# Kernel tuning notes

Measured on AMD Instinct MI355X. Metric: run time of the kernel, lower is better.

Reference implementation:

```python
import jax, jax.numpy as jnp
import numpy as np

B, S1, S2, H = 8, 2048, 2048, 1024

def setup_inputs() -> dict:
    key = jax.random.key(0)
    k1, k2, k3, k4, k5, k6 = jax.random.split(key, 6)
    value = jax.random.normal(k1, (B, S1, H), dtype=jnp.float32)
    key_t = jax.random.normal(k2, (B, S2, H), dtype=jnp.float32)
    query = jax.random.normal(k3, (B, S1, H), dtype=jnp.float32)
    mask = jax.random.randint(k4, (B, S1, S2), 0, 2).astype(jnp.bool_)
    # Linear(hidden, hidden) params, torch default init scale
    bound = 1.0 / np.sqrt(H)
    W = jax.random.uniform(k5, (H, H), minval=-bound, maxval=bound, dtype=jnp.float32)
    b = jax.random.uniform(k6, (H,), minval=-bound, maxval=bound, dtype=jnp.float32)
    return {"value": value, "key": key_t, "query": query, "mask": mask, "W": W, "b": b}

def reference(value, key, query, mask, W, b):
    # q_proj = query @ W^T + b  (torch Linear)
    q_proj = jnp.einsum('bqh,oh->bqo', query, W) + b            # [B,S1,H]
    attn = jnp.einsum('bqh,bkh->bqk', q_proj, key)               # [B,S1,S2]
    attn = jnp.where(mask, -jnp.inf, attn)
    attn = jnp.transpose(attn, (0, 2, 1))                        # [B,S2,S1]
    weights = jax.nn.softmax(attn, axis=-1)                      # softmax over S1
    context = jnp.einsum('bks,bsh->bkh', weights, value)         # [B,S2,H]
    return context, weights
```

## Files before the change

kernel.cpp:

```cpp
#include <hip/hip_runtime.h>

#define B_  8
#define S1_ 2048
#define S2_ 2048
#define H_  1024

typedef unsigned short u16;
typedef __attribute__((ext_vector_type(8))) short short8;
typedef __attribute__((ext_vector_type(4))) float f32x4;

__device__ __forceinline__ float b2f(u16 u) {
  union { unsigned int i; float f; } v; v.i = ((unsigned int)u) << 16; return v.f;
}
__device__ __forceinline__ u16 f2b(float f) {
  union { float f; unsigned int i; } v; v.f = f;
  unsigned int r = v.i + 0x7fffu + ((v.i >> 16) & 1u);
  return (u16)(r >> 16);
}

__device__ __forceinline__ int swz(int row, int kk) {
  return (row * 32 + kk) ^ (((row >> 1) & 3) << 3);
}

__device__ __forceinline__ void cvt8_split(float4 va, float4 vb, short8* hi, short8* lo) {
  float x[8] = {va.x, va.y, va.z, va.w, vb.x, vb.y, vb.z, vb.w};
  short8 h, l;
#pragma unroll
  for (int e = 0; e < 8; ++e) {
    u16 hb = f2b(x[e]);
    h[e] = (short)hb;
    l[e] = (short)f2b(x[e] - b2f(hb));
  }
  *hi = h; *lo = l;
}
__device__ __forceinline__ short8 cvt8(float4 va, float4 vb) {
  float x[8] = {va.x, va.y, va.z, va.w, vb.x, vb.y, vb.z, vb.w};
  short8 h;
#pragma unroll
  for (int e = 0; e < 8; ++e) h[e] = (short)f2b(x[e]);
  return h;
}

template<bool ADD_BIAS, bool DO_MASK, bool SPLIT, bool BTR>
__global__ __launch_bounds__(256)
void gemm_k(const float* __restrict__ A, long sA,
            const float* __restrict__ B, long sB, int ldb,
            const float* __restrict__ bias,
            const int* __restrict__ mask, long sMask, int mask_ld,
            float* __restrict__ C, long sC, int ldc, int K)
{
  __shared__ __align__(16) union {
    u16 tile[SPLIT ? 4 : 2][128 * 32];
    unsigned char m[128][128];
  } sh;

  const int t    = threadIdx.x;
  const int lane = t & 63;
  const int wv   = t >> 6;
  const int wm   = wv >> 1, wn = wv & 1;
  const int batch = blockIdx.z;
  const int m0 = blockIdx.x * 128;
  const int n0 = blockIdx.y * 128;

  const float* Ab = A + (long)batch * sA + (long)m0 * K;
  const float* Bb = B + (long)batch * sB + (BTR ? (long)n0 : (long)n0 * ldb);

  f32x4 acc[4][4];
#pragma unroll
  for (int i = 0; i < 4; ++i)
#pragma unroll
    for (int j = 0; j < 4; ++j)
      acc[i][j] = (f32x4){0.f, 0.f, 0.f, 0.f};

  const int c0 = t,       r0 = c0 >> 2, o0 = (c0 & 3) * 8;
  const int c1 = t + 256, r1 = c1 >> 2, o1 = (c1 & 3) * 8;

  const int fr = lane & 15;
  const int kg = lane >> 4;

  for (int kc = 0; kc < K; kc += 32) {
    float4 a00 = *(const float4*)(Ab + (long)r0 * K + kc + o0);
    float4 a01 = *(const float4*)(Ab + (long)r0 * K + kc + o0 + 4);
    float4 a10 = *(const float4*)(Ab + (long)r1 * K + kc + o1);
    float4 a11 = *(const float4*)(Ab + (long)r1 * K + kc + o1 + 4);
    float4 bb[4];
    float btv[2][8];
    if (BTR) {
#pragma unroll
      for (int p = 0; p < 2; ++p)
#pragma unroll
        for (int e = 0; e < 8; ++e)
          btv[p][e] = Bb[(long)(kc + wv * 8 + e) * ldb + lane + p * 64];
    } else {
      bb[0] = *(const float4*)(Bb + (long)r0 * ldb + kc + o0);
      bb[1] = *(const float4*)(Bb + (long)r0 * ldb + kc + o0 + 4);
      bb[2] = *(const float4*)(Bb + (long)r1 * ldb + kc + o1);
      bb[3] = *(const float4*)(Bb + (long)r1 * ldb + kc + o1 + 4);
    }
    __syncthreads();

    if (SPLIT) {
      short8 h, l;
      cvt8_split(a00, a01, &h, &l);
      *(short8*)&sh.tile[0][swz(r0, o0)] = h;  *(short8*)&sh.tile[2][swz(r0, o0)] = l;
      cvt8_split(a10, a11, &h, &l);
      *(short8*)&sh.tile[0][swz(r1, o1)] = h;  *(short8*)&sh.tile[2][swz(r1, o1)] = l;
      cvt8_split(bb[0], bb[1], &h, &l);
      *(short8*)&sh.tile[1][swz(r0, o0)] = h;  *(short8*)&sh.tile[3][swz(r0, o0)] = l;
      cvt8_split(bb[2], bb[3], &h, &l);
      *(short8*)&sh.tile[1][swz(r1, o1)] = h;  *(short8*)&sh.tile[3][swz(r1, o1)] = l;
    } else {
      *(short8*)&sh.tile[0][swz(r0, o0)] = cvt8(a00, a01);
      *(short8*)&sh.tile[0][swz(r1, o1)] = cvt8(a10, a11);
      if (BTR) {
#pragma unroll
        for (int p = 0; p < 2; ++p) {
          short8 h;
#pragma unroll
          for (int e = 0; e < 8; ++e) h[e] = (short)f2b(btv[p][e]);
          *(short8*)&sh.tile[1][swz(lane + p * 64, wv * 8)] = h;
        }
      } else {
        *(short8*)&sh.tile[1][swz(r0, o0)] = cvt8(bb[0], bb[1]);
        *(short8*)&sh.tile[1][swz(r1, o1)] = cvt8(bb[2], bb[3]);
      }
    }
    __syncthreads();

    short8 afh[4], bfh[4];
#pragma unroll
    for (int i = 0; i < 4; ++i)
      afh[i] = *(const short8*)&sh.tile[0][swz(wm * 64 + i * 16 + fr, kg * 8)];
#pragma unroll
    for (int j = 0; j < 4; ++j)
      bfh[j] = *(const short8*)&sh.tile[1][swz(wn * 64 + j * 16 + fr, kg * 8)];

    if (SPLIT) {
      short8 afl[4], bfl[4];
#pragma unroll
      for (int i = 0; i < 4; ++i)
        afl[i] = *(const short8*)&sh.tile[2][swz(wm * 64 + i * 16 + fr, kg * 8)];
#pragma unroll
      for (int j = 0; j < 4; ++j)
        bfl[j] = *(const short8*)&sh.tile[3][swz(wn * 64 + j * 16 + fr, kg * 8)];
#pragma unroll
      for (int i = 0; i < 4; ++i)
#pragma unroll
        for (int j = 0; j < 4; ++j) {
          acc[i][j] = __builtin_amdgcn_mfma_f32_16x16x32_bf16(afh[i], bfh[j], acc[i][j], 0, 0, 0);
          acc[i][j] = __builtin_amdgcn_mfma_f32_16x16x32_bf16(afh[i], bfl[j], acc[i][j], 0, 0, 0);
          acc[i][j] = __builtin_amdgcn_mfma_f32_16x16x32_bf16(afl[i], bfh[j], acc[i][j], 0, 0, 0);
        }
    } else {
#pragma unroll
      for (int i = 0; i < 4; ++i)
#pragma unroll
        for (int j = 0; j < 4; ++j)
          acc[i][j] = __builtin_amdgcn_mfma_f32_16x16x32_bf16(afh[i], bfh[j], acc[i][j], 0, 0, 0);
    }
  }

  if (DO_MASK) {
    __syncthreads();
    const int* mb = mask + (long)batch * sMask;
#pragma unroll
    for (int it = 0; it < 16; ++it) {
      int ql = it * 8 + (t >> 5);
      int kl = (t & 31) * 4;
      int4 mv = *(const int4*)(mb + (long)(n0 + ql) * mask_ld + (m0 + kl));
      sh.m[kl + 0][ql] = (unsigned char)(mv.x != 0);
      sh.m[kl + 1][ql] = (unsigned char)(mv.y != 0);
      sh.m[kl + 2][ql] = (unsigned char)(mv.z != 0);
      sh.m[kl + 3][ql] = (unsigned char)(mv.w != 0);
    }
    __syncthreads();
  }

  float bv[4];
  if (ADD_BIAS) {
#pragma unroll
    for (int j = 0; j < 4; ++j)
      bv[j] = bias[n0 + wn * 64 + j * 16 + fr];
  }

#pragma unroll
  for (int i = 0; i < 4; ++i) {
#pragma unroll
    for (int r = 0; r < 4; ++r) {
      int row = wm * 64 + i * 16 + (lane >> 4) * 4 + r;
      long gro = (long)batch * sC + (long)(m0 + row) * ldc + n0;
#pragma unroll
      for (int j = 0; j < 4; ++j) {
        int col = wn * 64 + j * 16 + fr;
        float v = acc[i][j][r];
        if (ADD_BIAS) v += bv[j];
        if (DO_MASK && sh.m[row][col]) v = -1e30f;
        C[gro + col] = v;
      }
    }
  }
}

__global__ __launch_bounds__(256)
void softmax_rows(float* __restrict__ scores)
{
  const long row = blockIdx.x;
  float* p = scores + row * (long)S1_;
  const int t = threadIdx.x;
  const int lane = t & 63, wv = t >> 6;

  float4 v0 = *(const float4*)(p + t * 8);
  float4 v1 = *(const float4*)(p + t * 8 + 4);
  float x[8] = {v0.x, v0.y, v0.z, v0.w, v1.x, v1.y, v1.z, v1.w};

  float m = x[0];
#pragma unroll
  for (int q = 1; q < 8; ++q) m = fmaxf(m, x[q]);
#pragma unroll
  for (int o = 32; o; o >>= 1) m = fmaxf(m, __shfl_xor(m, o));
  __shared__ float rb[4], sb[4];
  if (lane == 0) rb[wv] = m;
  __syncthreads();
  m = fmaxf(fmaxf(rb[0], rb[1]), fmaxf(rb[2], rb[3]));

  float e[8]; float s = 0.f;
#pragma unroll
  for (int q = 0; q < 8; ++q) { e[q] = __expf(x[q] - m); s += e[q]; }
#pragma unroll
  for (int o = 32; o; o >>= 1) s += __shfl_xor(s, o);
  if (lane == 0) sb[wv] = s;
  __syncthreads();
  s = sb[0] + sb[1] + sb[2] + sb[3];
  float inv = 1.f / s;

  float4 w0, w1;
  w0.x = e[0] * inv; w0.y = e[1] * inv; w0.z = e[2] * inv; w0.w = e[3] * inv;
  w1.x = e[4] * inv; w1.y = e[5] * inv; w1.z = e[6] * inv; w1.w = e[7] * inv;
  *(float4*)(p + t * 8)     = w0;
  *(float4*)(p + t * 8 + 4) = w1;
}

extern "C" void kernel_launch(void* const* d_in, const int* in_sizes, int n_in,
                              void* d_out, int out_size, void* d_ws, size_t ws_size,
                              hipStream_t stream)
{
  const float* value = (const float*)d_in[0];
  const float* key   = (const float*)d_in[1];
  const float* query = (const float*)d_in[2];
  const int*   mask  = (const int*)d_in[3];
  const float* W     = (const float*)d_in[4];
  const float* bias  = (const float*)d_in[5];

  float* ctx = (float*)d_out;
  float* wts = ctx + (size_t)B_ * S2_ * H_;
  float* qproj = ctx;

  dim3 blk(256);

  gemm_k<true, false, true, false><<<dim3((B_ * S1_) / 128, H_ / 128, 1), blk, 0, stream>>>(
      query, 0, W, 0, H_, bias, nullptr, 0, 0, qproj, 0, H_, H_);

  gemm_k<false, true, true, false><<<dim3(S2_ / 128, S1_ / 128, B_), blk, 0, stream>>>(
      key, (long)S2_ * H_, qproj, (long)S1_ * H_, H_, nullptr,
      mask, (long)S1_ * S2_, S2_, wts, (long)S2_ * S1_, S1_, H_);

  softmax_rows<<<dim3(B_ * S2_), blk, 0, stream>>>(wts);

  gemm_k<false, false, false, true><<<dim3(S2_ / 128, H_ / 128, B_), blk, 0, stream>>>(
      wts, (long)S2_ * S1_, value, (long)S1_ * H_, H_, nullptr,
      nullptr, 0, 0, ctx, (long)S2_ * H_, H_, S1_);
}
```

Measured before the change: 970.9 us.

## Pre-convert GEMM operands to bf16 hi/lo in workspace and load via global_load_lds

Result: faster. 950.4 us (-2.1%).

```diff
diff --git a/kernel.cpp b/kernel.cpp
--- a/kernel.cpp
+++ b/kernel.cpp
@@ -39,6 +39,154 @@
 #pragma unroll
   for (int e = 0; e < 8; ++e) h[e] = (short)f2b(x[e]);
   return h;
+}
+
+__device__ __forceinline__ void g2l16(const void* g, void* lds) {
+  __builtin_amdgcn_global_load_lds(
+      (const __attribute__((address_space(1))) unsigned int*)g,
+      (__attribute__((address_space(3))) unsigned int*)lds, 16, 0, 0);
+}
+
+template<bool ADD_BIAS, bool DO_MASK, bool SPLIT, bool OUTSPLIT>
+__global__ __launch_bounds__(256)
+void gemm_bf(const u16* __restrict__ Ahi, const u16* __restrict__ Alo, long sA, int lda,
+             const u16* __restrict__ Bhi, const u16* __restrict__ Blo, long sB, int ldb,
+             const float* __restrict__ bias,
+             const int* __restrict__ mask, long sMask, int mask_ld,
+             float* __restrict__ Cf, u16* __restrict__ Chi, u16* __restrict__ Clo,
+             long sC, int ldc, int K)
+{
+  __shared__ __align__(16) union {
+    u16 tile[SPLIT ? 4 : 2][128 * 32];
+    unsigned char m[128][128];
+  } sh;
+
+  const int t    = threadIdx.x;
+  const int lane = t & 63;
+  const int wv   = t >> 6;
+  const int wm   = wv >> 1, wn = wv & 1;
+  const int batch = blockIdx.z;
+  const int m0 = blockIdx.x * 128;
+  const int n0 = blockIdx.y * 128;
+
+  const u16* Ah = Ahi + (long)batch * sA + (long)m0 * lda;
+  const u16* Bh = Bhi + (long)batch * sB + (long)n0 * ldb;
+  const u16* Al = SPLIT ? (Alo + (long)batch * sA + (long)m0 * lda) : nullptr;
+  const u16* Bl = SPLIT ? (Blo + (long)batch * sB + (long)n0 * ldb) : nullptr;
+
+  f32x4 acc[4][4];
+#pragma unroll
+  for (int i = 0; i < 4; ++i)
+#pragma unroll
+    for (int j = 0; j < 4; ++j)
+      acc[i][j] = (f32x4){0.f, 0.f, 0.f, 0.f};
+
+  const int fr = lane & 15;
+  const int kg = lane >> 4;
+
+  int srow[2], soff[2], sdst[2];
+#pragma unroll
+  for (int half = 0; half < 2; ++half) {
+    int c = half * 256 + wv * 64 + lane;
+    int row = c >> 2;
+    srow[half] = row;
+    soff[half] = (((c & 3) ^ ((row >> 1) & 3)) * 8);
+    sdst[half] = (half * 256 + wv * 64) * 8;
+  }
+
+  for (int kc = 0; kc < K; kc += 32) {
+    __syncthreads();
+#pragma unroll
+    for (int half = 0; half < 2; ++half) {
+      const int ga = srow[half] * lda + kc + soff[half];
+      const int gb = srow[half] * ldb + kc + soff[half];
+      g2l16(Ah + ga, &sh.tile[0][sdst[half]]);
+      g2l16(Bh + gb, &sh.tile[1][sdst[half]]);
+      if (SPLIT) {
+        g2l16(Al + ga, &sh.tile[2][sdst[half]]);
+        g2l16(Bl + gb, &sh.tile[3][sdst[half]]);
+      }
+    }
+    __syncthreads();
+
+    short8 afh[4], bfh[4];
+#pragma unroll
+    for (int i = 0; i < 4; ++i)
+      afh[i] = *(const short8*)&sh.tile[0][swz(wm * 64 + i * 16 + fr, kg * 8)];
+#pragma unroll
+    for (int j = 0; j < 4; ++j)
+      bfh[j] = *(const short8*)&sh.tile[1][swz(wn * 64 + j * 16 + fr, kg * 8)];
+
+    if (SPLIT) {
+      short8 afl[4], bfl[4];
+#pragma unroll
+      for (int i = 0; i < 4; ++i)
+        afl[i] = *(const short8*)&sh.tile[2][swz(wm * 64 + i * 16 + fr, kg * 8)];
+#pragma unroll
+      for (int j = 0; j < 4; ++j)
+        bfl[j] = *(const short8*)&sh.tile[3][swz(wn * 64 + j * 16 + fr, kg * 8)];
+#pragma unroll
+      for (int i = 0; i < 4; ++i)
+#pragma unroll
+        for (int j = 0; j < 4; ++j) {
+          acc[i][j] = __builtin_amdgcn_mfma_f32_16x16x32_bf16(afh[i], bfh[j], acc[i][j], 0, 0, 0);
+          acc[i][j] = __builtin_amdgcn_mfma_f32_16x16x32_bf16(afh[i], bfl[j], acc[i][j], 0, 0, 0);
+          acc[i][j] = __builtin_amdgcn_mfma_f32_16x16x32_bf16(afl[i], bfh[j], acc[i][j], 0, 0, 0);
+        }
+    } else {
+#pragma unroll
+      for (int i = 0; i < 4; ++i)
+#pragma unroll
+        for (int j = 0; j < 4; ++j)
+          acc[i][j] = __builtin_amdgcn_mfma_f32_16x16x32_bf16(afh[i], bfh[j], acc[i][j], 0, 0, 0);
+    }
+  }
+
+  if (DO_MASK) {
+    __syncthreads();
+    const int* mb = mask + (long)batch * sMask;
+#pragma unroll
+    for (int it = 0; it < 16; ++it) {
+      int ql = it * 8 + (t >> 5);
+      int kl = (t & 31) * 4;
+      int4 mv = *(const int4*)(mb + (long)(n0 + ql) * mask_ld + (m0 + kl));
+      sh.m[kl + 0][ql] = (unsigned char)(mv.x != 0);
+      sh.m[kl + 1][ql] = (unsigned char)(mv.y != 0);
+      sh.m[kl + 2][ql] = (unsigned char)(mv.z != 0);
+      sh.m[kl + 3][ql] = (unsigned char)(mv.w != 0);
+    }
+    __syncthreads();
+  }
+
+  float bv[4];
+  if (ADD_BIAS) {
+#pragma unroll
+    for (int j = 0; j < 4; ++j)
+      bv[j] = bias[n0 + wn * 64 + j * 16 + fr];
+  }
+
+#pragma unroll
+  for (int i = 0; i < 4; ++i) {
+#pragma unroll
+    for (int r = 0; r < 4; ++r) {
+      int row = wm * 64 + i * 16 + (lane >> 4) * 4 + r;
+      long gro = (long)batch * sC + (long)(m0 + row) * ldc + n0;
+#pragma unroll
+      for (int j = 0; j < 4; ++j) {
+        int col = wn * 64 + j * 16 + fr;
+        float v = acc[i][j][r];
+        if (ADD_BIAS) v += bv[j];
+        if (OUTSPLIT) {
+          u16 hb = f2b(v);
+          Chi[gro + col] = hb;
+          Clo[gro + col] = f2b(v - b2f(hb));
+        } else {
+          if (DO_MASK && sh.m[row][col]) v = -1e30f;
+          Cf[gro + col] = v;
+        }
+      }
+    }
+  }
 }
 
 template<bool ADD_BIAS, bool DO_MASK, bool SPLIT, bool BTR>
@@ -202,7 +350,47 @@
 }
 
 __global__ __launch_bounds__(256)
-void softmax_rows(float* __restrict__ scores)
+void conv_split(const float* __restrict__ in, u16* __restrict__ hi, u16* __restrict__ lo)
+{
+  long i = ((long)blockIdx.x * 256 + threadIdx.x) * 8;
+  float4 v0 = *(const float4*)(in + i);
+  float4 v1 = *(const float4*)(in + i + 4);
+  short8 h, l;
+  cvt8_split(v0, v1, &h, &l);
+  *(short8*)(hi + i) = h;
+  *(short8*)(lo + i) = l;
+}
+
+__global__ __launch_bounds__(256)
+void transpose_conv(const float* __restrict__ v, u16* __restrict__ vt)
+{
+  __shared__ u16 tl[64][66];
+  const int b  = blockIdx.z;
+  const int s0 = blockIdx.x * 64, h0 = blockIdx.y * 64;
+  const int tr = threadIdx.x >> 4;
+  const int tc = (threadIdx.x & 15) * 4;
+  const float* vb = v + ((long)b * S1_ + s0) * H_ + h0;
+#pragma unroll
+  for (int q = 0; q < 4; ++q) {
+    int r = tr + q * 16;
+    float4 x = *(const float4*)(vb + (long)r * H_ + tc);
+    tl[r][tc + 0] = f2b(x.x); tl[r][tc + 1] = f2b(x.y);
+    tl[r][tc + 2] = f2b(x.z); tl[r][tc + 3] = f2b(x.w);
+  }
+  __syncthreads();
+  u16* ob = vt + ((long)b * H_ + h0) * S1_ + s0;
+#pragma unroll
+  for (int q = 0; q < 4; ++q) {
+    int hr = tr + q * 16;
+    unsigned int w0 = (unsigned int)tl[tc + 0][hr] | ((unsigned int)tl[tc + 1][hr] << 16);
+    unsigned int w1 = (unsigned int)tl[tc + 2][hr] | ((unsigned int)tl[tc + 3][hr] << 16);
+    uint2 w = {w0, w1};
+    *(uint2*)(ob + (long)hr * S1_ + tc) = w;
+  }
+}
+
+__global__ __launch_bounds__(256)
+void softmax_rows(float* __restrict__ scores, u16* __restrict__ wbf)
 {
   const long row = blockIdx.x;
   float* p = scores + row * (long)S1_;
@@ -233,11 +421,20 @@
   s = sb[0] + sb[1] + sb[2] + sb[3];
   float inv = 1.f / s;
 
-  float4 w0, w1;
-  w0.x = e[0] * inv; w0.y = e[1] * inv; w0.z = e[2] * inv; w0.w = e[3] * inv;
-  w1.x = e[4] * inv; w1.y = e[5] * inv; w1.z = e[6] * inv; w1.w = e[7] * inv;
-  *(float4*)(p + t * 8)     = w0;
-  *(float4*)(p + t * 8 + 4) = w1;
+  float w[8];
+#pragma unroll
+  for (int q = 0; q < 8; ++q) w[q] = e[q] * inv;
+  float4 o0 = {w[0], w[1], w[2], w[3]};
+  float4 o1 = {w[4], w[5], w[6], w[7]};
+  *(float4*)(p + t * 8)     = o0;
+  *(float4*)(p + t * 8 + 4) = o1;
+
+  if (wbf != nullptr) {
+    short8 hb;
+#pragma unroll
+    for (int q = 0; q < 8; ++q) hb[q] = (short)f2b(w[q]);
+    *(short8*)(wbf + row * (long)S1_ + t * 8) = hb;
+  }
 }
 
 extern "C" void kernel_launch(void* const* d_in, const int* in_sizes, int n_in,
@@ -253,20 +450,57 @@
 
   float* ctx = (float*)d_out;
   float* wts = ctx + (size_t)B_ * S2_ * H_;
-  float* qproj = ctx;
 
   dim3 blk(256);
-
-  gemm_k<true, false, true, false><<<dim3((B_ * S1_) / 128, H_ / 128, 1), blk, 0, stream>>>(
-      query, 0, W, 0, H_, bias, nullptr, 0, 0, qproj, 0, H_, H_);
-
-  gemm_k<false, true, true, false><<<dim3(S2_ / 128, S1_ / 128, B_), blk, 0, stream>>>(
-      key, (long)S2_ * H_, qproj, (long)S1_ * H_, H_, nullptr,
-      mask, (long)S1_ * S2_, S2_, wts, (long)S2_ * S1_, S1_, H_);
-
-  softmax_rows<<<dim3(B_ * S2_), blk, 0, stream>>>(wts);
-
-  gemm_k<false, false, false, true><<<dim3(S2_ / 128, H_ / 128, B_), blk, 0, stream>>>(
-      wts, (long)S2_ * S1_, value, (long)S1_ * H_, H_, nullptr,
-      nullptr, 0, 0, ctx, (long)S2_ * H_, H_, S1_);
-}
+  const size_t MB = 1024ull * 1024ull;
+
+  if (ws_size >= 132 * MB && d_ws != nullptr) {
+    u16* pjhi = (u16*)ctx;
+    u16* pjlo = (u16*)ctx + (size_t)B_ * S1_ * H_;
+
+    char* ws = (char*)d_ws;
+    u16* khi = (u16*)(ws);
+    u16* klo = (u16*)(ws + 32 * MB);
+    u16* wbf = (u16*)(ws);
+    u16* qhi = (u16*)(ws + 64 * MB);
+    u16* qlo = (u16*)(ws + 96 * MB);
+    u16* vT  = (u16*)(ws + 64 * MB);
+    u16* whi = (u16*)(ws + 128 * MB);
+    u16* wlo = (u16*)(ws + 130 * MB);
+
+    conv_split<<<dim3((B_ * S1_ * H_) / 2048), blk, 0, stream>>>(query, qhi, qlo);
+    conv_split<<<dim3((B_ * S2_ * H_) / 2048), blk, 0, stream>>>(key, khi, klo);
+    conv_split<<<dim3((H_ * H_) / 2048), blk, 0, stream>>>(W, whi, wlo);
+
+    gemm_bf<true, false, true, true><<<dim3((B_ * S1_) / 128, H_ / 128, 1), blk, 0, stream>>>(
+        qhi, qlo, 0, H_, whi, wlo, 0, H_, bias,
+        nullptr, 0, 0, nullptr, pjhi, pjlo, 0, H_, H_);
+
+    transpose_conv<<<dim3(S1_ / 64, H_ / 64, B_), blk, 0, stream>>>(value, vT);
+
+    gemm_bf<false, true, true, false><<<dim3(S2_ / 128, S1_ / 128, B_), blk, 0, stream>>>(
+        khi, klo, (long)S2_ * H_, H_, pjhi, pjlo, (long)S1_ * H_, H_, nullptr,
+        mask, (long)S1_ * S2_, S2_, wts, nullptr, nullptr, (long)S2_ * S1_, S1_, H_);
+
+    softmax_rows<<<dim3(B_ * S2_), blk, 0, stream>>>(wts, wbf);
+
+    gemm_bf<false, false, false, false><<<dim3(S2_ / 128, H_ / 128, B_), blk, 0, stream>>>(
+        wbf, nullptr, (long)S2_ * S1_, S1_, vT, nullptr, (long)H_ * S1_, S1_, nullptr,
+        nullptr, 0, 0, ctx, nullptr, nullptr, (long)S2_ * H_, H_, S1_);
+  } else {
+    float* qproj = ctx;
+
+    gemm_k<true, false, true, false><<<dim3((B_ * S1_) / 128, H_ / 128, 1), blk, 0, stream>>>(
+        query, 0, W, 0, H_, bias, nullptr, 0, 0, qproj, 0, H_, H_);
+
+    gemm_k<false, true, true, false><<<dim3(S2_ / 128, S1_ / 128, B_), blk, 0, stream>>>(
+        key, (long)S2_ * H_, qproj, (long)S1_ * H_, H_, nullptr,
+        mask, (long)S1_ * S2_, S2_, wts, (long)S2_ * S1_, S1_, H_);
+
+    softmax_rows<<<dim3(B_ * S2_), blk, 0, stream>>>(wts, nullptr);
+
+    gemm_k<false, false, false, true><<<dim3(S2_ / 128, H_ / 128, B_), blk, 0, stream>>>(
+        wts, (long)S2_ * S1_, value, (long)S1_ * H_, H_, nullptr,
+        nullptr, 0, 0, ctx, (long)S2_ * H_, H_, S1_);
+  }
+}
```
